# Performance work log

Hardware: AMD Instinct MI355X
Metric: run time of the kernel (lower is better)

The kernel has to match this reference:

```python
import jax, jax.numpy as jnp
import numpy as np

B, S, D_MODEL, H = 4, 1024, 768, 12
DEPTH = D_MODEL // H  # 64


def setup_inputs() -> dict:
    key = jax.random.key(0)
    ks = jax.random.split(key, 11)
    sd = 1.0 / np.sqrt(D_MODEL)
    return {
        "q": jax.random.normal(ks[0], (B, S, D_MODEL), jnp.float32),
        "k": jax.random.normal(ks[1], (B, S, D_MODEL), jnp.float32),
        "v": jax.random.normal(ks[2], (B, S, D_MODEL), jnp.float32),
        # NOTE: source uses [Dense(depth)] * num_heads -> ONE shared layer per q/k/v
        "Wq": jax.random.normal(ks[3], (D_MODEL, DEPTH), jnp.float32) * sd,
        "bq": jnp.zeros((DEPTH,), jnp.float32),
        "Wk": jax.random.normal(ks[4], (D_MODEL, DEPTH), jnp.float32) * sd,
        "bk": jnp.zeros((DEPTH,), jnp.float32),
        "Wv": jax.random.normal(ks[5], (D_MODEL, DEPTH), jnp.float32) * sd,
        "bv": jnp.zeros((DEPTH,), jnp.float32),
        "Wc": jax.random.normal(ks[6], (D_MODEL, D_MODEL), jnp.float32) * sd,
        "bc": jnp.zeros((D_MODEL,), jnp.float32),
    }


def reference(q, k, v, Wq, bq, Wk, bk, Wv, bv, Wc, bc):
    # All heads share the same weights (list * num_heads aliasing in source),
    # so compute one head and replicate. Heads produce identical outputs.
    qh = q @ Wq + bq  # [B, S, depth]
    kh = k @ Wk + bk
    vh = v @ Wv + bv
    # Source bug reproduced: dk = tf.shape(k)[1] on [B,H,S,depth] == num_heads
    scale = 1.0 / jnp.sqrt(jnp.float32(H))
    scores = jnp.einsum('bqd,bkd->bqk', qh, kh) * scale  # [B, S, S]
    weights = jax.nn.softmax(scores, axis=-1)
    oh = jnp.einsum('bqk,bkd->bqd', weights, vh)  # [B, S, depth]
    # concat of H identical heads along feature dim -> tile
    concat = jnp.tile(oh, (1, 1, H))  # [B, S, d_model]
    output = concat @ Wc + bc
    attention_weights = jnp.broadcast_to(weights[:, None], (B, H, S, S))
    return (output, attention_weights)
```

## Files before the change

kernel.cpp:

```cpp
#include <hip/hip_runtime.h>
#include <math.h>

#define BB 4
#define SS 1024
#define DM 768
#define HH 12
#define DEPTH 64
#define QBLK 8
#define PROWS 16
#define NROWS (BB * SS)

typedef float vfloat4 __attribute__((ext_vector_type(4)));
typedef short bf16x8 __attribute__((ext_vector_type(8)));
typedef float f32x4 __attribute__((ext_vector_type(4)));

__device__ inline ushort f2bf(float x) {
    uint u = __float_as_uint(x);
    u += 0x7FFFu + ((u >> 16) & 1u);
    return (ushort)(u >> 16);
}

__global__ __launch_bounds__(256, 3) void proj_kernel(
    const float* __restrict__ q, const float* __restrict__ k, const float* __restrict__ v,
    const float* __restrict__ Wq, const float* __restrict__ bq,
    const float* __restrict__ Wk, const float* __restrict__ bk,
    const float* __restrict__ Wv, const float* __restrict__ bv,
    float* __restrict__ qh, ushort* __restrict__ khu, ushort* __restrict__ vhu)
{
    __shared__ __align__(16) float rows[PROWS][DM];
    const int nrb  = NROWS / PROWS;
    const int m    = blockIdx.x / nrb;
    const int rb   = blockIdx.x % nrb;
    const int row0 = rb * PROWS;
    const int t    = threadIdx.x;

    const float* src  = (m == 0) ? q  : (m == 1) ? k  : v;
    const float* W    = (m == 0) ? Wq : (m == 1) ? Wk : Wv;
    const float* bias = (m == 0) ? bq : (m == 1) ? bk : bv;

    const float4* s4 = (const float4*)(src + (size_t)row0 * DM);
    float4* r4 = (float4*)&rows[0][0];
    for (int i = t; i < PROWS * DM / 4; i += 256) r4[i] = s4[i];
    __syncthreads();

    const int d  = t & 63;
    const int rg = t >> 6;
    const float* Wp = W + d;
    float a0 = bias[d], a1 = a0, a2 = a0, a3 = a0;
    #pragma unroll 8
    for (int i = 0; i < DM; i += 4) {
        const float wv0 = Wp[(size_t)(i + 0) * DEPTH];
        const float wv1 = Wp[(size_t)(i + 1) * DEPTH];
        const float wv2 = Wp[(size_t)(i + 2) * DEPTH];
        const float wv3 = Wp[(size_t)(i + 3) * DEPTH];
        const float4 r0 = *(const float4*)&rows[rg * 4 + 0][i];
        const float4 r1 = *(const float4*)&rows[rg * 4 + 1][i];
        const float4 r2 = *(const float4*)&rows[rg * 4 + 2][i];
        const float4 r3 = *(const float4*)&rows[rg * 4 + 3][i];
        a0 = fmaf(r0.x, wv0, a0); a0 = fmaf(r0.y, wv1, a0); a0 = fmaf(r0.z, wv2, a0); a0 = fmaf(r0.w, wv3, a0);
        a1 = fmaf(r1.x, wv0, a1); a1 = fmaf(r1.y, wv1, a1); a1 = fmaf(r1.z, wv2, a1); a1 = fmaf(r1.w, wv3, a1);
        a2 = fmaf(r2.x, wv0, a2); a2 = fmaf(r2.y, wv1, a2); a2 = fmaf(r2.z, wv2, a2); a2 = fmaf(r2.w, wv3, a2);
        a3 = fmaf(r3.x, wv0, a3); a3 = fmaf(r3.y, wv1, a3); a3 = fmaf(r3.z, wv2, a3); a3 = fmaf(r3.w, wv3, a3);
    }
    const size_t base = (size_t)(row0 + rg * 4) * DEPTH + d;
    if (m == 0) {
        float* dp = qh + base;
        dp[0] = a0; dp[DEPTH] = a1; dp[2 * DEPTH] = a2; dp[3 * DEPTH] = a3;
    } else {
        ushort* du = ((m == 1) ? khu : vhu) + base;
        du[0] = f2bf(a0); du[DEPTH] = f2bf(a1); du[2 * DEPTH] = f2bf(a2); du[3 * DEPTH] = f2bf(a3);
    }
}

__global__ __launch_bounds__(256) void wcred_kernel(
    const float* __restrict__ Wc, float* __restrict__ Wr)
{
    int idx = blockIdx.x * 256 + threadIdx.x;
    if (idx >= DEPTH * DM) return;
    int d = idx / DM, j = idx % DM;
    float s = 0.f;
    #pragma unroll
    for (int h = 0; h < HH; ++h)
        s += Wc[(size_t)(h * DEPTH + d) * DM + j];
    Wr[idx] = s;
}

__global__ __launch_bounds__(512, 4) void attn_core(
    const float* __restrict__ qh, const ushort* __restrict__ khu, const ushort* __restrict__ vhu,
    const float* __restrict__ Wr, const float* __restrict__ bc,
    float* __restrict__ out, float* __restrict__ attn)
{
    __shared__ __align__(16) ushort qf[16 * 72];
    __shared__ __align__(16) ushort kvbuf[256 * 72];
    __shared__ __align__(16) ushort pf[16 * 1032];
    __shared__ float redmax[16 * 8];
    __shared__ float redsum[16 * 8];

    const int t = threadIdx.x, l = t & 63, wid = t >> 6;
    const int li = l & 15, g4 = l >> 4;
    const int blk = blockIdx.x, b = blk >> 7;
    const int q0 = (blk & 127) * QBLK;

    {
        const int qq = t >> 6, dd = t & 63;
        qf[qq * 72 + dd] = f2bf(qh[((size_t)b * SS + q0 + qq) * DEPTH + dd] * 0.28867513459481287f);
        for (int i = t; i < 8 * 72; i += 512) qf[8 * 72 + i] = 0;
        for (int i = t; i < 8 * 1032; i += 512) pf[8 * 1032 + i] = 0;
    }
    __syncthreads();

    const bf16x8 a0 = *(const bf16x8*)&qf[li * 72 + g4 * 8];
    const bf16x8 a1 = *(const bf16x8*)&qf[li * 72 + 32 + g4 * 8];

    f32x4 c[8];
    #pragma unroll
    for (int i = 0; i < 8; ++i) c[i] = (f32x4){0.f, 0.f, 0.f, 0.f};

    const ushort* khb = khu + (size_t)b * SS * DEPTH;
    #pragma unroll
    for (int s = 0; s < 4; ++s) {
        {
            const int key = t >> 1, hf = t & 1;
            const uint4* g = (const uint4*)(khb + (size_t)(s * 256 + key) * DEPTH + hf * 32);
            uint4 r0 = g[0], r1 = g[1], r2 = g[2], r3 = g[3];
            uint4* d4 = (uint4*)&kvbuf[key * 72 + hf * 32];
            d4[0] = r0; d4[1] = r1; d4[2] = r2; d4[3] = r3;
        }
        __syncthreads();
        #pragma unroll
        for (int jj = 0; jj < 2; ++jj) {
            const int tl = wid + 8 * jj;
            const int ci = 2 * s + jj;
            const bf16x8 b0 = *(const bf16x8*)&kvbuf[(tl * 16 + li) * 72 + g4 * 8];
            const bf16x8 b1 = *(const bf16x8*)&kvbuf[(tl * 16 + li) * 72 + 32 + g4 * 8];
            c[ci] = __builtin_amdgcn_mfma_f32_16x16x32_bf16(a0, b0, c[ci], 0, 0, 0);
            c[ci] = __builtin_amdgcn_mfma_f32_16x16x32_bf16(a1, b1, c[ci], 0, 0, 0);
        }
        __syncthreads();
    }

    float mx[4], sm[4], inv[4];
    #pragma unroll
    for (int r = 0; r < 4; ++r) {
        float m_ = c[0][r];
        #pragma unroll
        for (int i = 1; i < 8; ++i) m_ = fmaxf(m_, c[i][r]);
        #pragma unroll
        for (int off = 1; off < 16; off <<= 1) m_ = fmaxf(m_, __shfl_xor(m_, off));
        mx[r] = m_;
    }
    if (li == 0) {
        #pragma unroll
        for (int r = 0; r < 4; ++r) redmax[(4 * g4 + r) * 8 + wid] = mx[r];
    }
    __syncthreads();
    #pragma unroll
    for (int r = 0; r < 4; ++r) {
        float m_ = redmax[(4 * g4 + r) * 8];
        #pragma unroll
        for (int w2 = 1; w2 < 8; ++w2) m_ = fmaxf(m_, redmax[(4 * g4 + r) * 8 + w2]);
        mx[r] = m_;
        sm[r] = 0.f;
    }
    #pragma unroll
    for (int i = 0; i < 8; ++i) {
        #pragma unroll
        for (int r = 0; r < 4; ++r) {
            const float e = __expf(c[i][r] - mx[r]);
            c[i][r] = e;
            sm[r] += e;
        }
    }
    #pragma unroll
    for (int r = 0; r < 4; ++r) {
        float s_ = sm[r];
        #pragma unroll
        for (int off = 1; off < 16; off <<= 1) s_ += __shfl_xor(s_, off);
        sm[r] = s_;
    }
    if (li == 0) {
        #pragma unroll
        for (int r = 0; r < 4; ++r) redsum[(4 * g4 + r) * 8 + wid] = sm[r];
    }
    __syncthreads();
    #pragma unroll
    for (int r = 0; r < 4; ++r) {
        float s_ = 0.f;
        #pragma unroll
        for (int w2 = 0; w2 < 8; ++w2) s_ += redsum[(4 * g4 + r) * 8 + w2];
        inv[r] = 1.f / s_;
    }
    if (l < 32) {
        #pragma unroll
        for (int i = 0; i < 8; ++i) {
            const int colbase = (16 * (i >> 1) + wid + 8 * (i & 1)) * 16 + li;
            #pragma unroll
            for (int r = 0; r < 4; ++r)
                pf[(4 * g4 + r) * 1032 + colbase] = f2bf(c[i][r] * inv[r]);
        }
    }
    __syncthreads();

    f32x4 cp = {0.f, 0.f, 0.f, 0.f};
    const int dt = wid >> 1, par = wid & 1;
    const ushort* vhb = vhu + (size_t)b * SS * DEPTH;
    ushort* VT = kvbuf;
    #pragma unroll
    for (int s = 0; s < 4; ++s) {
        {
            const int kk = t & 255, dh = t >> 8, d0 = dh * 32;
            const bf16x8* g = (const bf16x8*)(vhb + (size_t)(s * 256 + kk) * DEPTH + d0);
            const bf16x8 v0 = g[0], v1 = g[1], v2 = g[2], v3 = g[3];
            #pragma unroll
            for (int i = 0; i < 8; ++i) {
                VT[(d0 + i     ) * 264 + kk] = (ushort)v0[i];
                VT[(d0 + 8 + i ) * 264 + kk] = (ushort)v1[i];
                VT[(d0 + 16 + i) * 264 + kk] = (ushort)v2[i];
                VT[(d0 + 24 + i) * 264 + kk] = (ushort)v3[i];
            }
        }
        __syncthreads();
        #pragma unroll
        for (int c2 = 0; c2 < 4; ++c2) {
            const int cc = par + 2 * c2;
            const bf16x8 ap = *(const bf16x8*)&pf[li * 1032 + s * 256 + cc * 32 + g4 * 8];
            const bf16x8 bv = *(const bf16x8*)&VT[(dt * 16 + li) * 264 + cc * 32 + g4 * 8];
            cp = __builtin_amdgcn_mfma_f32_16x16x32_bf16(ap, bv, cp, 0, 0, 0);
        }
        __syncthreads();
    }

    float* part_f = (float*)kvbuf;
    float* ohT_f  = ((float*)kvbuf) + 2048;
    #pragma unroll
    for (int r = 0; r < 4; ++r) part_f[wid * 256 + r * 64 + l] = cp[r];
    __syncthreads();
    {
        const int qq = t >> 6, dd = t & 63;
        const int ls = (qq >> 2) * 16 + (dd & 15), rr = qq & 3, w0 = (dd >> 4) * 2;
        ohT_f[dd * 12 + qq] = part_f[w0 * 256 + rr * 64 + ls] + part_f[(w0 + 1) * 256 + rr * 64 + ls];
    }
    __syncthreads();

    for (int j = t; j < DM; j += 512) {
        float a[QBLK];
        const float bj = bc[j];
        #pragma unroll
        for (int r = 0; r < QBLK; ++r) a[r] = bj;
        const float* wc = Wr + j;
        #pragma unroll 16
        for (int d2 = 0; d2 < DEPTH; ++d2) {
            const float wv = wc[(size_t)d2 * DM];
            const float4 o0 = *(const float4*)&ohT_f[d2 * 12];
            const float4 o1 = *(const float4*)&ohT_f[d2 * 12 + 4];
            a[0] = fmaf(o0.x, wv, a[0]); a[1] = fmaf(o0.y, wv, a[1]);
            a[2] = fmaf(o0.z, wv, a[2]); a[3] = fmaf(o0.w, wv, a[3]);
            a[4] = fmaf(o1.x, wv, a[4]); a[5] = fmaf(o1.y, wv, a[5]);
            a[6] = fmaf(o1.z, wv, a[6]); a[7] = fmaf(o1.w, wv, a[7]);
        }
        float* ob = out + ((size_t)b * SS + q0) * DM + j;
        #pragma unroll
        for (int r = 0; r < QBLK; ++r)
            __builtin_nontemporal_store(a[r], ob + (size_t)r * DM);
    }

    {
        const int qq = t >> 6, c0 = t & 63;
        float* a0p = attn + (((size_t)b * HH) * SS + (q0 + qq)) * SS;
        #pragma unroll
        for (int i = 0; i < 16; ++i) {
            const int col = c0 + 64 * i;
            const float val = __uint_as_float((uint)pf[qq * 1032 + col] << 16);
            __builtin_nontemporal_store(val, a0p + col);
        }
    }
}

#define BROWS 2
__global__ __launch_bounds__(256) void bcast_kernel(float* __restrict__ attn)
{
    const int t = threadIdx.x;
    #pragma unroll
    for (int r = 0; r < BROWS; ++r) {
        const int gr = blockIdx.x * BROWS + r;
        const int b  = gr >> 10;
        const int qi = gr & (SS - 1);
        float* base = attn + (((size_t)b * HH) * SS + qi) * SS;
        const vfloat4 val = ((const vfloat4*)base)[t];
        #pragma unroll
        for (int h = 1; h < HH; ++h)
            __builtin_nontemporal_store(val, (vfloat4*)(base + (size_t)h * SS * SS) + t);
    }
}

extern "C" void kernel_launch(void* const* d_in, const int* in_sizes, int n_in,
                              void* d_out, int out_size, void* d_ws, size_t ws_size,
                              hipStream_t stream) {
    const float* q  = (const float*)d_in[0];
    const float* k  = (const float*)d_in[1];
    const float* v  = (const float*)d_in[2];
    const float* Wq = (const float*)d_in[3];
    const float* bq = (const float*)d_in[4];
    const float* Wk = (const float*)d_in[5];
    const float* bk = (const float*)d_in[6];
    const float* Wv = (const float*)d_in[7];
    const float* bv = (const float*)d_in[8];
    const float* Wc = (const float*)d_in[9];
    const float* bc = (const float*)d_in[10];

    float* out  = (float*)d_out;
    float* attn = out + (size_t)BB * SS * DM;

    float* ws = (float*)d_ws;
    const size_t NPROJ = (size_t)NROWS * DEPTH;
    float* qh   = ws;
    ushort* khu = (ushort*)(ws + NPROJ);
    ushort* vhu = (ushort*)(ws + NPROJ + NPROJ / 2);
    float* Wr   = ws + 2 * NPROJ;

    proj_kernel<<<3 * (NROWS / PROWS), 256, 0, stream>>>(q, k, v, Wq, bq, Wk, bk, Wv, bv, qh, khu, vhu);
    wcred_kernel<<<(DEPTH * DM + 255) / 256, 256, 0, stream>>>(Wc, Wr);
    attn_core<<<BB * (SS / QBLK), 512, 0, stream>>>(qh, khu, vhu, Wr, bc, out, attn);
    bcast_kernel<<<NROWS / BROWS, 256, 0, stream>>>(attn);
}
```

Measured before the change: 107.7 us.

## Prefetch next K/V tile into registers and raise MFMA wave priority

The K and V tile loops now issue the global loads for the next 256-key tile into registers before the current tile's MFMAs run. Global latency overlaps compute, and one barrier per iteration is dropped. The MFMA sections are wrapped in s_setprio, and the first V tile load is hoisted ahead of the softmax. The attention-weight store is moved before the output projection so its writes start earlier. This raises register pressure under launch_bounds(512,4), which could cause spills or lower occupancy.

```diff
diff --git a/kernel.cpp b/kernel.cpp
--- a/kernel.cpp
+++ b/kernel.cpp
@@ -100,6 +100,7 @@
     const int li = l & 15, g4 = l >> 4;
     const int blk = blockIdx.x, b = blk >> 7;
     const int q0 = (blk & 127) * QBLK;
+    const int key = t >> 1, hf = t & 1;
 
     {
         const int qq = t >> 6, dd = t & 63;
@@ -107,6 +108,15 @@
         for (int i = t; i < 8 * 72; i += 512) qf[8 * 72 + i] = 0;
         for (int i = t; i < 8 * 1032; i += 512) pf[8 * 1032 + i] = 0;
     }
+
+    const ushort* khb = khu + (size_t)b * SS * DEPTH;
+    const ushort* vhb = vhu + (size_t)b * SS * DEPTH;
+
+    uint4 kr0, kr1, kr2, kr3;
+    {
+        const uint4* g = (const uint4*)(khb + (size_t)key * DEPTH + hf * 32);
+        kr0 = g[0]; kr1 = g[1]; kr2 = g[2]; kr3 = g[3];
+    }
     __syncthreads();
 
     const bf16x8 a0 = *(const bf16x8*)&qf[li * 72 + g4 * 8];
@@ -116,17 +126,19 @@
     #pragma unroll
     for (int i = 0; i < 8; ++i) c[i] = (f32x4){0.f, 0.f, 0.f, 0.f};
 
-    const ushort* khb = khu + (size_t)b * SS * DEPTH;
     #pragma unroll
     for (int s = 0; s < 4; ++s) {
+        if (s) __syncthreads();
         {
-            const int key = t >> 1, hf = t & 1;
-            const uint4* g = (const uint4*)(khb + (size_t)(s * 256 + key) * DEPTH + hf * 32);
-            uint4 r0 = g[0], r1 = g[1], r2 = g[2], r3 = g[3];
             uint4* d4 = (uint4*)&kvbuf[key * 72 + hf * 32];
-            d4[0] = r0; d4[1] = r1; d4[2] = r2; d4[3] = r3;
+            d4[0] = kr0; d4[1] = kr1; d4[2] = kr2; d4[3] = kr3;
+        }
+        if (s < 3) {
+            const uint4* g = (const uint4*)(khb + (size_t)((s + 1) * 256 + key) * DEPTH + hf * 32);
+            kr0 = g[0]; kr1 = g[1]; kr2 = g[2]; kr3 = g[3];
         }
         __syncthreads();
+        __builtin_amdgcn_s_setprio(1);
         #pragma unroll
         for (int jj = 0; jj < 2; ++jj) {
             const int tl = wid + 8 * jj;
@@ -136,7 +148,13 @@
             c[ci] = __builtin_amdgcn_mfma_f32_16x16x32_bf16(a0, b0, c[ci], 0, 0, 0);
             c[ci] = __builtin_amdgcn_mfma_f32_16x16x32_bf16(a1, b1, c[ci], 0, 0, 0);
         }
-        __syncthreads();
+        __builtin_amdgcn_s_setprio(0);
+    }
+
+    bf16x8 vr0, vr1, vr2, vr3;
+    {
+        const bf16x8* g = (const bf16x8*)(vhb + (size_t)key * DEPTH + hf * 32);
+        vr0 = g[0]; vr1 = g[1]; vr2 = g[2]; vr3 = g[3];
     }
 
     float mx[4], sm[4], inv[4];
@@ -203,23 +221,25 @@
 
     f32x4 cp = {0.f, 0.f, 0.f, 0.f};
     const int dt = wid >> 1, par = wid & 1;
-    const ushort* vhb = vhu + (size_t)b * SS * DEPTH;
     ushort* VT = kvbuf;
     #pragma unroll
     for (int s = 0; s < 4; ++s) {
+        if (s) __syncthreads();
         {
-            const int kk = t & 255, dh = t >> 8, d0 = dh * 32;
-            const bf16x8* g = (const bf16x8*)(vhb + (size_t)(s * 256 + kk) * DEPTH + d0);
-            const bf16x8 v0 = g[0], v1 = g[1], v2 = g[2], v3 = g[3];
             #pragma unroll
             for (int i = 0; i < 8; ++i) {
-                VT[(d0 + i     ) * 264 + kk] = (ushort)v0[i];
-                VT[(d0 + 8 + i ) * 264 + kk] = (ushort)v1[i];
-                VT[(d0 + 16 + i) * 264 + kk] = (ushort)v2[i];
-                VT[(d0 + 24 + i) * 264 + kk] = (ushort)v3[i];
+                VT[(hf * 32 + i     ) * 264 + key] = (ushort)vr0[i];
+                VT[(hf * 32 + 8 + i ) * 264 + key] = (ushort)vr1[i];
+                VT[(hf * 32 + 16 + i) * 264 + key] = (ushort)vr2[i];
+                VT[(hf * 32 + 24 + i) * 264 + key] = (ushort)vr3[i];
             }
         }
+        if (s < 3) {
+            const bf16x8* g = (const bf16x8*)(vhb + (size_t)((s + 1) * 256 + key) * DEPTH + hf * 32);
+            vr0 = g[0]; vr1 = g[1]; vr2 = g[2]; vr3 = g[3];
+        }
         __syncthreads();
+        __builtin_amdgcn_s_setprio(1);
         #pragma unroll
         for (int c2 = 0; c2 < 4; ++c2) {
             const int cc = par + 2 * c2;
@@ -227,8 +247,9 @@
             const bf16x8 bv = *(const bf16x8*)&VT[(dt * 16 + li) * 264 + cc * 32 + g4 * 8];
             cp = __builtin_amdgcn_mfma_f32_16x16x32_bf16(ap, bv, cp, 0, 0, 0);
         }
-        __syncthreads();
-    }
+        __builtin_amdgcn_s_setprio(0);
+    }
+    __syncthreads();
 
     float* part_f = (float*)kvbuf;
     float* ohT_f  = ((float*)kvbuf) + 2048;
@@ -241,6 +262,17 @@
         ohT_f[dd * 12 + qq] = part_f[w0 * 256 + rr * 64 + ls] + part_f[(w0 + 1) * 256 + rr * 64 + ls];
     }
     __syncthreads();
+
+    {
+        const int qq = t >> 6, c0 = t & 63;
+        float* a0p = attn + (((size_t)b * HH) * SS + (q0 + qq)) * SS;
+        #pragma unroll
+        for (int i = 0; i < 16; ++i) {
+            const int col = c0 + 64 * i;
+            const float val = __uint_as_float((uint)pf[qq * 1032 + col] << 16);
+            __builtin_nontemporal_store(val, a0p + col);
+        }
+    }
 
     for (int j = t; j < DM; j += 512) {
         float a[QBLK];
@@ -262,17 +294,6 @@
         #pragma unroll
         for (int r = 0; r < QBLK; ++r)
             __builtin_nontemporal_store(a[r], ob + (size_t)r * DM);
-    }
-
-    {
-        const int qq = t >> 6, c0 = t & 63;
-        float* a0p = attn + (((size_t)b * HH) * SS + (q0 + qq)) * SS;
-        #pragma unroll
-        for (int i = 0; i < 16; ++i) {
-            const int col = c0 + 64 * i;
-            const float val = __uint_as_float((uint)pf[qq * 1032 + col] << 16);
-            __builtin_nontemporal_store(val, a0p + col);
-        }
     }
 }
 
```

After: 105.3 us. 1.02x faster.

## Write V transposed in projection and feed MFMA operands directly from global

Applied to the files above, without the earlier changes.

The projection kernel now writes V in a transposed [depth][rows] bf16 layout via a shared-memory transpose. The attention kernel then drops the LDS staging of K and V and its barriers, loading MFMA B operands straight from global/L2. It also splits the PV accumulator in two, raises wave priority around the MFMA loops, and moves the attention-weights store ahead of the output projection so the big write starts earlier. This trades LDS traffic and syncs for uncoalesced-ish direct global loads that rely on cache hits.

```diff
diff --git a/kernel.cpp b/kernel.cpp
--- a/kernel.cpp
+++ b/kernel.cpp
@@ -25,9 +25,10 @@
     const float* __restrict__ Wq, const float* __restrict__ bq,
     const float* __restrict__ Wk, const float* __restrict__ bk,
     const float* __restrict__ Wv, const float* __restrict__ bv,
-    float* __restrict__ qh, ushort* __restrict__ khu, ushort* __restrict__ vhu)
+    float* __restrict__ qh, ushort* __restrict__ khu, ushort* __restrict__ vhT)
 {
     __shared__ __align__(16) float rows[PROWS][DM];
+    __shared__ float resT[DEPTH][PROWS + 1];
     const int nrb  = NROWS / PROWS;
     const int m    = blockIdx.x / nrb;
     const int rb   = blockIdx.x % nrb;
@@ -62,13 +63,23 @@
         a2 = fmaf(r2.x, wv0, a2); a2 = fmaf(r2.y, wv1, a2); a2 = fmaf(r2.z, wv2, a2); a2 = fmaf(r2.w, wv3, a2);
         a3 = fmaf(r3.x, wv0, a3); a3 = fmaf(r3.y, wv1, a3); a3 = fmaf(r3.z, wv2, a3); a3 = fmaf(r3.w, wv3, a3);
     }
-    const size_t base = (size_t)(row0 + rg * 4) * DEPTH + d;
-    if (m == 0) {
-        float* dp = qh + base;
+    if (m == 2) {
+        resT[d][rg * 4 + 0] = a0;
+        resT[d][rg * 4 + 1] = a1;
+        resT[d][rg * 4 + 2] = a2;
+        resT[d][rg * 4 + 3] = a3;
+        __syncthreads();
+        #pragma unroll
+        for (int e = t; e < DEPTH * PROWS; e += 256) {
+            const int dd = e >> 4, rr = e & 15;
+            vhT[(size_t)dd * NROWS + row0 + rr] = f2bf(resT[dd][rr]);
+        }
+    } else if (m == 1) {
+        ushort* du = khu + (size_t)(row0 + rg * 4) * DEPTH + d;
+        du[0] = f2bf(a0); du[DEPTH] = f2bf(a1); du[2 * DEPTH] = f2bf(a2); du[3 * DEPTH] = f2bf(a3);
+    } else {
+        float* dp = qh + (size_t)(row0 + rg * 4) * DEPTH + d;
         dp[0] = a0; dp[DEPTH] = a1; dp[2 * DEPTH] = a2; dp[3 * DEPTH] = a3;
-    } else {
-        ushort* du = ((m == 1) ? khu : vhu) + base;
-        du[0] = f2bf(a0); du[DEPTH] = f2bf(a1); du[2 * DEPTH] = f2bf(a2); du[3 * DEPTH] = f2bf(a3);
     }
 }
 
@@ -86,15 +97,16 @@
 }
 
 __global__ __launch_bounds__(512, 4) void attn_core(
-    const float* __restrict__ qh, const ushort* __restrict__ khu, const ushort* __restrict__ vhu,
+    const float* __restrict__ qh, const ushort* __restrict__ khu, const ushort* __restrict__ vhT,
     const float* __restrict__ Wr, const float* __restrict__ bc,
     float* __restrict__ out, float* __restrict__ attn)
 {
     __shared__ __align__(16) ushort qf[16 * 72];
-    __shared__ __align__(16) ushort kvbuf[256 * 72];
     __shared__ __align__(16) ushort pf[16 * 1032];
     __shared__ float redmax[16 * 8];
     __shared__ float redsum[16 * 8];
+    __shared__ __align__(16) float part_f[8 * 256];
+    __shared__ __align__(16) float ohT_f[64 * 12];
 
     const int t = threadIdx.x, l = t & 63, wid = t >> 6;
     const int li = l & 15, g4 = l >> 4;
@@ -117,27 +129,21 @@
     for (int i = 0; i < 8; ++i) c[i] = (f32x4){0.f, 0.f, 0.f, 0.f};
 
     const ushort* khb = khu + (size_t)b * SS * DEPTH;
+    __builtin_amdgcn_s_setprio(1);
     #pragma unroll
     for (int s = 0; s < 4; ++s) {
-        {
-            const int key = t >> 1, hf = t & 1;
-            const uint4* g = (const uint4*)(khb + (size_t)(s * 256 + key) * DEPTH + hf * 32);
-            uint4 r0 = g[0], r1 = g[1], r2 = g[2], r3 = g[3];
-            uint4* d4 = (uint4*)&kvbuf[key * 72 + hf * 32];
-            d4[0] = r0; d4[1] = r1; d4[2] = r2; d4[3] = r3;
-        }
-        __syncthreads();
         #pragma unroll
         for (int jj = 0; jj < 2; ++jj) {
-            const int tl = wid + 8 * jj;
+            const int tile = s * 16 + wid + 8 * jj;
             const int ci = 2 * s + jj;
-            const bf16x8 b0 = *(const bf16x8*)&kvbuf[(tl * 16 + li) * 72 + g4 * 8];
-            const bf16x8 b1 = *(const bf16x8*)&kvbuf[(tl * 16 + li) * 72 + 32 + g4 * 8];
+            const ushort* kp = khb + (size_t)(tile * 16 + li) * DEPTH + g4 * 8;
+            const bf16x8 b0 = *(const bf16x8*)kp;
+            const bf16x8 b1 = *(const bf16x8*)(kp + 32);
             c[ci] = __builtin_amdgcn_mfma_f32_16x16x32_bf16(a0, b0, c[ci], 0, 0, 0);
             c[ci] = __builtin_amdgcn_mfma_f32_16x16x32_bf16(a1, b1, c[ci], 0, 0, 0);
         }
-        __syncthreads();
-    }
+    }
+    __builtin_amdgcn_s_setprio(0);
 
     float mx[4], sm[4], inv[4];
     #pragma unroll
@@ -201,37 +207,25 @@
     }
     __syncthreads();
 
-    f32x4 cp = {0.f, 0.f, 0.f, 0.f};
     const int dt = wid >> 1, par = wid & 1;
-    const ushort* vhb = vhu + (size_t)b * SS * DEPTH;
-    ushort* VT = kvbuf;
+    const ushort* vtb = vhT + (size_t)b * SS;
+    f32x4 cp0 = {0.f, 0.f, 0.f, 0.f}, cp1 = {0.f, 0.f, 0.f, 0.f};
+    __builtin_amdgcn_s_setprio(1);
     #pragma unroll
     for (int s = 0; s < 4; ++s) {
-        {
-            const int kk = t & 255, dh = t >> 8, d0 = dh * 32;
-            const bf16x8* g = (const bf16x8*)(vhb + (size_t)(s * 256 + kk) * DEPTH + d0);
-            const bf16x8 v0 = g[0], v1 = g[1], v2 = g[2], v3 = g[3];
-            #pragma unroll
-            for (int i = 0; i < 8; ++i) {
-                VT[(d0 + i     ) * 264 + kk] = (ushort)v0[i];
-                VT[(d0 + 8 + i ) * 264 + kk] = (ushort)v1[i];
-                VT[(d0 + 16 + i) * 264 + kk] = (ushort)v2[i];
-                VT[(d0 + 24 + i) * 264 + kk] = (ushort)v3[i];
-            }
-        }
-        __syncthreads();
         #pragma unroll
         for (int c2 = 0; c2 < 4; ++c2) {
             const int cc = par + 2 * c2;
-            const bf16x8 ap = *(const bf16x8*)&pf[li * 1032 + s * 256 + cc * 32 + g4 * 8];
-            const bf16x8 bv = *(const bf16x8*)&VT[(dt * 16 + li) * 264 + cc * 32 + g4 * 8];
-            cp = __builtin_amdgcn_mfma_f32_16x16x32_bf16(ap, bv, cp, 0, 0, 0);
-        }
-        __syncthreads();
-    }
-
-    float* part_f = (float*)kvbuf;
-    float* ohT_f  = ((float*)kvbuf) + 2048;
+            const int kk = s * 256 + cc * 32 + g4 * 8;
+            const bf16x8 ap = *(const bf16x8*)&pf[li * 1032 + kk];
+            const bf16x8 bv = *(const bf16x8*)(vtb + (size_t)(dt * 16 + li) * NROWS + kk);
+            if (s & 1) cp1 = __builtin_amdgcn_mfma_f32_16x16x32_bf16(ap, bv, cp1, 0, 0, 0);
+            else       cp0 = __builtin_amdgcn_mfma_f32_16x16x32_bf16(ap, bv, cp0, 0, 0, 0);
+        }
+    }
+    __builtin_amdgcn_s_setprio(0);
+    const f32x4 cp = cp0 + cp1;
+
     #pragma unroll
     for (int r = 0; r < 4; ++r) part_f[wid * 256 + r * 64 + l] = cp[r];
     __syncthreads();
@@ -241,6 +235,17 @@
         ohT_f[dd * 12 + qq] = part_f[w0 * 256 + rr * 64 + ls] + part_f[(w0 + 1) * 256 + rr * 64 + ls];
     }
     __syncthreads();
+
+    {
+        const int qq = t >> 6, c0 = t & 63;
+        float* a0p = attn + (((size_t)b * HH) * SS + (q0 + qq)) * SS;
+        #pragma unroll
+        for (int i = 0; i < 16; ++i) {
+            const int col = c0 + 64 * i;
+            const float val = __uint_as_float((uint)pf[qq * 1032 + col] << 16);
+            __builtin_nontemporal_store(val, a0p + col);
+        }
+    }
 
     for (int j = t; j < DM; j += 512) {
         float a[QBLK];
@@ -262,17 +267,6 @@
         #pragma unroll
         for (int r = 0; r < QBLK; ++r)
             __builtin_nontemporal_store(a[r], ob + (size_t)r * DM);
-    }
-
-    {
-        const int qq = t >> 6, c0 = t & 63;
-        float* a0p = attn + (((size_t)b * HH) * SS + (q0 + qq)) * SS;
-        #pragma unroll
-        for (int i = 0; i < 16; ++i) {
-            const int col = c0 + 64 * i;
-            const float val = __uint_as_float((uint)pf[qq * 1032 + col] << 16);
-            __builtin_nontemporal_store(val, a0p + col);
-        }
     }
 }
 
@@ -315,11 +309,11 @@
     const size_t NPROJ = (size_t)NROWS * DEPTH;
     float* qh   = ws;
     ushort* khu = (ushort*)(ws + NPROJ);
-    ushort* vhu = (ushort*)(ws + NPROJ + NPROJ / 2);
+    ushort* vhT = (ushort*)(ws + NPROJ + NPROJ / 2);
     float* Wr   = ws + 2 * NPROJ;
 
-    proj_kernel<<<3 * (NROWS / PROWS), 256, 0, stream>>>(q, k, v, Wq, bq, Wk, bk, Wv, bv, qh, khu, vhu);
+    proj_kernel<<<3 * (NROWS / PROWS), 256, 0, stream>>>(q, k, v, Wq, bq, Wk, bk, Wv, bv, qh, khu, vhT);
     wcred_kernel<<<(DEPTH * DM + 255) / 256, 256, 0, stream>>>(Wc, Wr);
-    attn_core<<<BB * (SS / QBLK), 512, 0, stream>>>(qh, khu, vhu, Wr, bc, out, attn);
+    attn_core<<<BB * (SS / QBLK), 512, 0, stream>>>(qh, khu, vhT, Wr, bc, out, attn);
     bcast_kernel<<<NROWS / BROWS, 256, 0, stream>>>(attn);
 }
```

Result: slower. 112.0 us (+4.0%).
